# Kernel tuning notes

Hardware: AMD Instinct MI355X
Metric: run time of the kernel (lower is better)

## Reference

```python
import jax, jax.numpy as jnp
import numpy as np

B, D, FD, HW, NH, NC = 8, 384, 256, 64, 8, 4
NP = HW * HW
HD = D // NH


def _ln(x, g, b, eps=1e-5):
    m = jnp.mean(x, -1, keepdims=True)
    v = jnp.mean((x - m) ** 2, -1, keepdims=True)
    return (x - m) / jnp.sqrt(v + eps) * g + b


def _grn(x, g, b, eps=1e-6):
    # x: [B, D, H, W]; global L2 norm per channel over spatial dims
    gx = jnp.sqrt(jnp.sum(x * x, axis=(-2, -1), keepdims=True))  # [B,D,1,1]
    nx = gx / (jnp.mean(gx, axis=-3, keepdims=True) + eps)
    return (1.0 + g[:, None, None]) * (x * nx) + b[:, None, None] + x


def _adaln(x, film, W, bW, g, b):
    gb = film @ W.T + bW                       # [B, 2D]
    gamma, beta = jnp.split(gb, 2, axis=-1)
    return _grn(x, g, b) * (1.0 + gamma)[:, :, None, None] + beta[:, :, None, None]


def setup_inputs() -> dict:
    ks = jax.random.split(jax.random.key(0), 24)
    n = lambda k, s: jax.random.normal(k, s, jnp.float32)
    w = lambda k, o, i: n(k, (o, i)) * 0.02
    return {
        "image": n(ks[0], (B, D, HW, HW)),
        "film_vector": n(ks[1], (B, FD)),
        "perm": jax.random.permutation(ks[2], NP).astype(jnp.int32),
        "Wq": w(ks[3], D, D), "bq": jnp.zeros(D),
        "Wk": w(ks[4], D, D), "bk": jnp.zeros(D),
        "Wv": w(ks[5], D, D), "bv": jnp.zeros(D),
        "Wo": w(ks[6], D, D), "bo": jnp.zeros(D),
        "lnq_g": jnp.ones(D), "lnq_b": jnp.zeros(D),
        "lnk_g": jnp.ones(D), "lnk_b": jnp.zeros(D),
        "ada1_W": n(ks[7], (2 * D, FD)) * 0.001, "ada1_b": jnp.zeros(2 * D),
        "grn1_g": jnp.zeros(D), "grn1_b": jnp.zeros(D),
        "ada2_W": n(ks[8], (2 * D, FD)) * 0.001, "ada2_b": jnp.zeros(2 * D),
        "grn2_g": jnp.zeros(D), "grn2_b": jnp.zeros(D),
        "conv1_W": w(ks[9], 4 * D, D), "conv1_b": jnp.zeros(4 * D),
        "conv2_W": w(ks[10], D, 4 * D), "conv2_b": jnp.zeros(D),
        "cloud_scalar": jnp.ones(D),
        "ffn_scalar": jnp.ones(D),
        "final_scalar": jnp.ones(D) * 0.1,
        "num_clouds": NC,
    }


def reference(image, film_vector, perm, Wq, bq, Wk, bk, Wv, bv, Wo, bo,
              lnq_g, lnq_b, lnk_g, lnk_b, ada1_W, ada1_b, grn1_g, grn1_b,
              ada2_W, ada2_b, grn2_g, grn2_b, conv1_W, conv1_b, conv2_W, conv2_b,
              cloud_scalar, ffn_scalar, final_scalar, num_clouds):
    b, d, h, w = image.shape
    tp = h * w
    gs = tp // num_clouds

    # ---- cloud attention branch ----
    x = _adaln(image, film_vector, ada1_W, ada1_b, grn1_g, grn1_b)
    x_sh = x.reshape(b, d, tp)[:, :, perm]                       # shuffled pixels
    xg = x_sh.transpose(0, 2, 1).reshape(b * num_clouds, gs, d)  # [b*nc, gs, d]

    q = _ln(xg @ Wq.T + bq, lnq_g, lnq_b)
    k = _ln(xg @ Wk.T + bk, lnk_g, lnk_b)
    v = (xg @ Wv.T + bv).reshape(-1, gs, NH, HD)
    q = jax.nn.elu(q.reshape(-1, gs, NH, HD)) + 1.0
    k = jax.nn.elu(k.reshape(-1, gs, NH, HD)) + 1.0

    kv = jnp.einsum('bnhd,bnhe->bhde', k, v)                 # [b*nc, H, hd, hd]
    ksum = k.sum(axis=1)                                      # [b*nc, H, hd]
    num = jnp.einsum('bqhd,bhde->bqhe', q, kv)
    den = jnp.einsum('bqhd,bhd->bqh', q, ksum)[..., None] + 1e-8
    ao = (num / den).reshape(-1, gs, d) @ Wo.T + bo           # [b*nc, gs, d]

    ao = ao.reshape(b, num_clouds, gs, d).transpose(0, 3, 1, 2).reshape(b, d, tp)
    inv_perm = jnp.argsort(perm)
    ao = ao[:, :, inv_perm].reshape(b, d, h, w)

    wi = image + ao * cloud_scalar[:, None, None]

    # ---- FFN branch (1x1 convs) ----
    x2 = _adaln(wi, film_vector, ada2_W, ada2_b, grn2_g, grn2_b)
    h1 = jax.nn.silu(jnp.einsum('bdhw,ed->behw', x2, conv1_W) + conv1_b[:, None, None])
    fo = jnp.einsum('behw,de->bdhw', h1, conv2_W) + conv2_b[:, None, None]
    wi = wi + fo * ffn_scalar[:, None, None]

    return image + wi * final_scalar[:, None, None]
```

## Files before the change

kernel.cpp:

```cpp
#include <hip/hip_runtime.h>
#include <hip/hip_bf16.h>
#include <math.h>

#define BB      8
#define DD      384
#define FDIM    256
#define NPIX    4096
#define NHEAD   8
#define NCLOUD  4
#define HDIM    48
#define GSZ     1024
#define TT      (BB*NPIX)
#define DHID    (4*DD)
#define TD      1152

typedef __hip_bfloat16 bf16;
typedef __attribute__((ext_vector_type(8))) short bf16x8;
typedef __attribute__((ext_vector_type(4))) float f32x4;
typedef __attribute__((ext_vector_type(2))) unsigned int u32x2;

__device__ __forceinline__ float b2f(bf16 x){ return __bfloat162float(x); }
__device__ __forceinline__ bf16  f2b(float x){ return __float2bfloat16(x); }
__device__ __forceinline__ float lo2f(unsigned u){ union{unsigned i; float f;} c; c.i = u << 16; return c.f; }
__device__ __forceinline__ float hi2f(unsigned u){ union{unsigned i; float f;} c; c.i = u & 0xffff0000u; return c.f; }
__device__ __forceinline__ unsigned short f2bs(float x){ bf16 b = f2b(x); return *(unsigned short*)&b; }
__device__ __forceinline__ unsigned pack2(float a, float b){
    return (unsigned)f2bs(a) | ((unsigned)f2bs(b) << 16);
}

#if defined(__has_builtin)
#if __has_builtin(__builtin_amdgcn_global_load_lds)
#define USE_GLL 1
#endif
#endif
#ifndef USE_GLL
#define USE_GLL 0
#endif

typedef __attribute__((address_space(1))) void gas_t;
typedef __attribute__((address_space(3))) void las_t;
__device__ __forceinline__ void gload16(const void* g, void* l){
#if USE_GLL
    __builtin_amdgcn_global_load_lds((gas_t*)(void*)g, (las_t*)l, 16, 0, 0);
#else
    *(bf16x8*)l = *(const bf16x8*)g;
#endif
}

__device__ __forceinline__ float block_sum(float v, float* sm, int nthreads){
    #pragma unroll
    for (int o = 32; o > 0; o >>= 1) v += __shfl_down(v, o, 64);
    int nw = nthreads >> 6;
    __syncthreads();
    if ((threadIdx.x & 63) == 0) sm[threadIdx.x >> 6] = v;
    __syncthreads();
    float s = sm[0];
    for (int i = 1; i < nw; i++) s += sm[i];
    return s;
}

#define WSEG 147456
#define WBIG 589824
__global__ void prologue(const float* Wq, const float* Wk, const float* Wv, const float* Wo,
                         const float* W1, const float* W2, bf16* wb,
                         const float* film, const float* ada1_W, const float* ada1_b,
                         const float* ada2_W, const float* ada2_b, float* gb1, float* gb2,
                         const int* perm, int* invp,
                         const float* bq, const float* bk, const float* bv, float* bqkv,
                         float* gxsq, float* gxsq2){
    int blk = blockIdx.x, tid = threadIdx.x;
    if (blk < 6912){
        int i = blk*256 + tid;
        float v;
        if      (i <   WSEG) v = Wq[i];
        else if (i < 2*WSEG) v = Wk[i -   WSEG];
        else if (i < 3*WSEG) v = Wv[i - 2*WSEG];
        else if (i < 4*WSEG) v = Wo[i - 3*WSEG];
        else if (i < 4*WSEG + WBIG) v = W1[i - 4*WSEG];
        else v = W2[i - 4*WSEG - WBIG];
        wb[i] = f2b(v);
    } else if (blk < 6960){
        int idx = (blk-6912)*256 + tid;
        int which = idx / (BB*768);
        int r = idx % (BB*768);
        int bb = r / 768, j = r % 768;
        const float* W = which ? ada2_W : ada1_W;
        const float* bi = which ? ada2_b : ada1_b;
        const float* f = film + bb*FDIM;
        const float* w = W + (size_t)j*FDIM;
        float s = 0.f;
        for (int i = 0; i < FDIM; i++) s += f[i]*w[i];
        (which ? gb2 : gb1)[bb*768 + j] = s + bi[j];
    } else if (blk < 6976){
        int i = (blk-6960)*256 + tid;
        if (i < NPIX) invp[perm[i]] = i;
    } else if (blk < 6981){
        int i = (blk-6976)*256 + tid;
        if (i < 384) bqkv[i] = bq[i];
        else if (i < 768) bqkv[i] = bk[i-384];
        else if (i < 1152) bqkv[i] = bv[i-768];
    } else {
        int i = (blk-6981)*256 + tid;
        if (i < BB*DD){ gxsq[i] = 0.f; gxsq2[i] = 0.f; }
    }
}

__global__ void prep1(const float* img, bf16* imgT, float* gxsq){
    __shared__ float tile[32][33];
    __shared__ float red[32][8];
    int b = blockIdx.z, p0 = blockIdx.x*32, d0 = blockIdx.y*32;
    int tx = threadIdx.x, ty = threadIdx.y;
    #pragma unroll
    for (int i = 0; i < 32; i += 8)
        tile[ty+i][tx] = img[((size_t)b*DD + d0+ty+i)*NPIX + p0+tx];
    __syncthreads();
    #pragma unroll
    for (int i = 0; i < 32; i += 8){
        int p = p0 + ty + i;
        imgT[((size_t)(b<<12) + p)*DD + d0+tx] = f2b(tile[tx][ty+i]);
    }
    float s = 0.f;
    #pragma unroll
    for (int k = 0; k < 4; k++){ float v = tile[tx][ty*4 + k]; s += v*v; }
    red[tx][ty] = s;
    __syncthreads();
    if (ty == 0){
        float t2 = 0.f;
        #pragma unroll
        for (int k = 0; k < 8; k++) t2 += red[tx][k];
        atomicAdd(&gxsq[b*DD + d0+tx], t2);
    }
}

template<bool SQ>
__global__ void grn_nx(const float* gin, float* nx){
    __shared__ float sm[6];
    int b = blockIdx.x; int d = threadIdx.x;
    float g = gin[b*DD + d];
    if (SQ) g = sqrtf(g);
    float tot = block_sum(g, sm, 384);
    nx[b*DD + d] = g / (tot/(float)DD + 1e-6f);
}

__global__ __launch_bounds__(256) void adaln1_tok(const bf16* imgT, const float* nx,
                        const float* gg, const float* gbv, const float* gb,
                        const int* invp, bf16* xt){
    int t = blockIdx.x*4 + (threadIdx.x >> 6);
    int lane = threadIdx.x & 63;
    int b = t >> 12, p = t & 4095;
    int j = invp[p];
    const unsigned* src = (const unsigned*)(imgT + (size_t)t*DD);
    unsigned* dst = (unsigned*)(xt + ((size_t)(b<<12) + j)*DD);
    int d0 = lane*6;
    const float* nxp = nx + b*DD + d0;
    const float* g1 = gb + b*768 + d0;
    const float* g2 = gb + b*768 + 384 + d0;
    #pragma unroll
    for (int i = 0; i < 3; i++){
        unsigned u = src[lane*3 + i];
        float v0 = lo2f(u), v1 = hi2f(u);
        int dd0 = 2*i, dd1 = 2*i+1;
        float r0 = ((1.f + gg[d0+dd0])*(v0*nxp[dd0]) + gbv[d0+dd0] + v0)*(1.f + g1[dd0]) + g2[dd0];
        float r1 = ((1.f + gg[d0+dd1])*(v1*nxp[dd1]) + gbv[d0+dd1] + v1)*(1.f + g1[dd1]) + g2[dd1];
        dst[lane*3 + i] = pack2(r0, r1);
    }
}

__global__ __launch_bounds__(256) void adaln2_tok(const bf16* wi, const float* nx,
                        const float* gg, const float* gbv, const float* gb, bf16* xout){
    int t = blockIdx.x*4 + (threadIdx.x >> 6);
    int lane = threadIdx.x & 63;
    int b = t >> 12;
    const unsigned* src = (const unsigned*)(wi + (size_t)t*DD);
    unsigned* dst = (unsigned*)(xout + (size_t)t*DD);
    int d0 = lane*6;
    const float* nxp = nx + b*DD + d0;
    const float* g1 = gb + b*768 + d0;
    const float* g2 = gb + b*768 + 384 + d0;
    #pragma unroll
    for (int i = 0; i < 3; i++){
        unsigned u = src[lane*3 + i];
        float v0 = lo2f(u), v1 = hi2f(u);
        int dd0 = 2*i, dd1 = 2*i+1;
        float r0 = ((1.f + gg[d0+dd0])*(v0*nxp[dd0]) + gbv[d0+dd0] + v0)*(1.f + g1[dd0]) + g2[dd0];
        float r1 = ((1.f + gg[d0+dd1])*(v1*nxp[dd1]) + gbv[d0+dd1] + v1)*(1.f + g1[dd1]) + g2[dd1];
        dst[lane*3 + i] = pack2(r0, r1);
    }
}

template<int EPI>
__global__ __launch_bounds__(256, 2) void gemm_mfma(const bf16* __restrict__ A,
                          const bf16* __restrict__ W,
                          const float* __restrict__ bias,
                          bf16* __restrict__ C,
                          int M, int N, int K, const int* __restrict__ rowmap,
                          const bf16* __restrict__ imgT, const float* __restrict__ csc){
    __shared__ short lds_[36864];
    int tid  = threadIdx.x;
    int lane = tid & 63, wid = tid >> 6;
    int quad = lane >> 4, l16 = lane & 15;
    int wm = (wid >> 1) * 128, wn = (wid & 1) * 64;

    int v = blockIdx.y * gridDim.x + blockIdx.x;
    int xcd = v & 7, ii = v >> 3;
    int nby = gridDim.y;
    int by = xcd * (nby >> 3) + ii / gridDim.x;
    int bx = ii % gridDim.x;
    int m0 = by * 256, n0 = bx * 128;

    const bf16* sp[6]; int lof[6];
    #pragma unroll
    for (int it = 0; it < 6; it++){
        int s = tid + it*256;
        int half = s >> 10;
        int r = (s >> 2) & (half ? 127 : 255);
        int seg = (s & 3) ^ ((s >> 3) & 3);
        sp[it] = (half ? W + (size_t)(n0 + r)*K : A + (size_t)(m0 + r)*K) + seg*8;
        lof[it] = s*8;
    }
    int xorv = (quad ^ ((l16 >> 1) & 3)) * 8;

    int nk = K >> 5;
    #pragma unroll
    for (int it = 0; it < 6; it++) gload16(sp[it], lds_ + lof[it]);
    #pragma unroll
    for (int it = 0; it < 6; it++) gload16(sp[it] + 32, lds_ + 12288 + lof[it]);

    f32x4 acc[8][4] = {};
    for (int k = 0; k < nk; k++){
        if (k < nk-1) asm volatile("s_waitcnt vmcnt(6)" ::: "memory");
        else          asm volatile("s_waitcnt vmcnt(0)" ::: "memory");
        __builtin_amdgcn_s_barrier();
        __builtin_amdgcn_sched_barrier(0);
        if (k + 2 < nk){
            int koff = (k+2) * 32;
            int boff = ((k+2) % 3) * 12288;
            #pragma unroll
            for (int it = 0; it < 6; it++) gload16(sp[it] + koff, lds_ + boff + lof[it]);
        }
        const short* base = lds_ + (k % 3) * 12288;
        const short* a_ = base + (wm + l16)*32 + xorv;
        const short* w_ = base + 8192 + (wn + l16)*32 + xorv;
        bf16x8 af[8], wf[4];
        #pragma unroll
        for (int t = 0; t < 8; t++) af[t] = *(const bf16x8*)(void*)(a_ + t*512);
        #pragma unroll
        for (int t = 0; t < 4; t++) wf[t] = *(const bf16x8*)(void*)(w_ + t*512);
        #pragma unroll
        for (int i = 0; i < 8; i++)
            #pragma unroll
            for (int j2 = 0; j2 < 4; j2++)
                acc[i][j2] = __builtin_amdgcn_mfma_f32_16x16x32_bf16(wf[j2], af[i], acc[i][j2], 0, 0, 0);
    }
    int nbase = n0 + wn + quad*4;
    f32x4 bsv[4], csv[4];
    #pragma unroll
    for (int j2 = 0; j2 < 4; j2++) bsv[j2] = *(const f32x4*)(bias + nbase + j2*16);
    if (EPI == 2){
        #pragma unroll
        for (int j2 = 0; j2 < 4; j2++) csv[j2] = *(const f32x4*)(csc + nbase + j2*16);
    }
    #pragma unroll
    for (int i = 0; i < 8; i++){
        int row = m0 + wm + i*16 + l16;
        int grow = rowmap ? ((row & ~4095) | rowmap[row & 4095]) : row;
        bf16* cp = C + (size_t)grow*N + nbase;
        const bf16* ip = imgT + (size_t)grow*DD + nbase;
        #pragma unroll
        for (int j2 = 0; j2 < 4; j2++){
            float v0 = acc[i][j2][0] + bsv[j2][0];
            float v1 = acc[i][j2][1] + bsv[j2][1];
            float v2 = acc[i][j2][2] + bsv[j2][2];
            float v3 = acc[i][j2][3] + bsv[j2][3];
            if (EPI == 1){
                v0 = v0 / (1.f + __expf(-v0));
                v1 = v1 / (1.f + __expf(-v1));
                v2 = v2 / (1.f + __expf(-v2));
                v3 = v3 / (1.f + __expf(-v3));
            }
            if (EPI == 2){
                u32x2 iw = *(const u32x2*)(void*)(ip + j2*16);
                v0 = lo2f(iw.x) + v0*csv[j2][0];
                v1 = hi2f(iw.x) + v1*csv[j2][1];
                v2 = lo2f(iw.y) + v2*csv[j2][2];
                v3 = hi2f(iw.y) + v3*csv[j2][3];
            }
            u32x2 st;
            st.x = pack2(v0, v1);
            st.y = pack2(v2, v3);
            *(u32x2*)(void*)(cp + j2*16) = st;
        }
    }
}

__global__ __launch_bounds__(256) void ln_elu_qk(bf16* qkv,
                        const float* gq, const float* bq2,
                        const float* gk, const float* bk2){
    int r = blockIdx.x*4 + (threadIdx.x >> 6);
    int lane = threadIdx.x & 63;
    int t = r >> 1, which = r & 1;
    unsigned* row32 = (unsigned*)(qkv + (size_t)t*TD + which*384);
    const float* g = which ? gk : gq;
    const float* b = which ? bk2 : bq2;
    unsigned u[3];
    #pragma unroll
    for (int i = 0; i < 3; i++) u[i] = row32[lane*3 + i];
    float vv[6];
    #pragma unroll
    for (int i = 0; i < 3; i++){ vv[2*i] = lo2f(u[i]); vv[2*i+1] = hi2f(u[i]); }
    float s = 0.f;
    #pragma unroll
    for (int i = 0; i < 6; i++) s += vv[i];
    #pragma unroll
    for (int o = 32; o > 0; o >>= 1) s += __shfl_xor(s, o, 64);
    float mean = s / (float)DD;
    float s2 = 0.f;
    #pragma unroll
    for (int i = 0; i < 6; i++){ float d = vv[i]-mean; s2 += d*d; }
    #pragma unroll
    for (int o = 32; o > 0; o >>= 1) s2 += __shfl_xor(s2, o, 64);
    float rstd = rsqrtf(s2/(float)DD + 1e-5f);
    int d0 = lane*6;
    #pragma unroll
    for (int i = 0; i < 3; i++){
        float y0 = (vv[2*i]-mean)*rstd*g[d0+2*i] + b[d0+2*i];
        float y1 = (vv[2*i+1]-mean)*rstd*g[d0+2*i+1] + b[d0+2*i+1];
        y0 = (y0 > 0.f) ? y0 : expm1f(y0);
        y1 = (y1 > 0.f) ? y1 : expm1f(y1);
        row32[lane*3 + i] = pack2(y0 + 1.f, y1 + 1.f);
    }
}

__global__ __launch_bounds__(256) void kv_ksum_part(const bf16* qkv, float* kvp, float* ksp){
    int bch = blockIdx.x >> 3, sub = blockIdx.x & 7;
    int bc = bch >> 3, h = bch & 7;
    __shared__ float ks[16][49];
    __shared__ float vs[16][49];
    int eg = (threadIdx.x >> 4) * 3;
    int fg = (threadIdx.x & 15) * 3;
    float acc[3][3] = {};
    float ksacc[3] = {};
    int nbase = bc*GSZ + sub*128;
    for (int n0 = 0; n0 < 128; n0 += 16){
        for (int i = threadIdx.x; i < 16*48; i += 256){
            int n = i/48, e = i%48;
            size_t base = (size_t)(nbase + n0 + n)*TD + h*HDIM;
            ks[n][e] = b2f(qkv[base + 384 + e]);
            vs[n][e] = b2f(qkv[base + 768 + e]);
        }
        __syncthreads();
        #pragma unroll 4
        for (int n = 0; n < 16; n++){
            float ka[3], vb[3];
            #pragma unroll
            for (int i = 0; i < 3; i++){ ka[i] = ks[n][eg+i]; vb[i] = vs[n][fg+i]; }
            #pragma unroll
            for (int i = 0; i < 3; i++)
                #pragma unroll
                for (int j = 0; j < 3; j++)
                    acc[i][j] += ka[i]*vb[j];
            if ((threadIdx.x & 15) == 0){
                #pragma unroll
                for (int i = 0; i < 3; i++) ksacc[i] += ka[i];
            }
        }
        __syncthreads();
    }
    float* kvo = kvp + (size_t)blockIdx.x*2304;
    #pragma unroll
    for (int i = 0; i < 3; i++)
        #pragma unroll
        for (int j = 0; j < 3; j++)
            kvo[(eg+i)*48 + fg+j] = acc[i][j];
    if ((threadIdx.x & 15) == 0){
        #pragma unroll
        for (int i = 0; i < 3; i++) ksp[(size_t)blockIdx.x*48 + eg+i] = ksacc[i];
    }
}

__global__ void kv_reduce(const float* kvp, const float* ksp, float* kv, float* ksum){
    int idx = blockIdx.x*256 + threadIdx.x;
    if (idx < 256*2304){
        int bch = idx / 2304, r = idx - bch*2304;
        const float* p = kvp + (size_t)bch*8*2304 + r;
        float s = 0.f;
        #pragma unroll
        for (int u = 0; u < 8; u++) s += p[u*2304];
        kv[idx] = s;
    } else if (idx < 256*2304 + 256*48){
        int k2 = idx - 256*2304;
        int bch = k2 / 48, r = k2 - bch*48;
        const float* p = ksp + (size_t)bch*8*48 + r;
        float s = 0.f;
        #pragma unroll
        for (int u = 0; u < 8; u++) s += p[u*48];
        ksum[k2] = s;
    }
}

__global__ __launch_bounds__(256) void attn_apply(const bf16* __restrict__ qkv,
                                                  const float* __restrict__ kv,
                                                  const float* __restrict__ ksum,
                                                  bf16* __restrict__ out){
    __shared__ __align__(16) bf16 Wm[64][72];
    int bch = blockIdx.x >> 2, rs = blockIdx.x & 3;
    int bc = bch >> 3, h = bch & 7;
    int tid = threadIdx.x;
    int lane = tid & 63, w = tid >> 6;
    int l16 = lane & 15, quad = lane >> 4;

    for (int i = tid; i < 64*72; i += 256) ((unsigned short*)Wm)[i] = 0;
    __syncthreads();
    const float* kvh = kv + (size_t)bch*(HDIM*HDIM);
    for (int i = tid; i < HDIM*HDIM; i += 256){
        int e = i / HDIM, f = i - e*HDIM;
        Wm[f][e] = f2b(kvh[i]);
    }
    if (tid < HDIM) Wm[HDIM][tid] = f2b(ksum[(size_t)bch*HDIM + tid]);
    __syncthreads();

    bf16x8 bw[4][2];
    #pragma unroll
    for (int n = 0; n < 4; n++){
        bw[n][0] = *(const bf16x8*)(void*)&Wm[n*16 + l16][quad*8];
        bw[n][1] = *(const bf16x8*)(void*)&Wm[n*16 + l16][32 + quad*8];
    }

    int rowbase0 = bc*GSZ + rs*256 + w*64;
    #pragma unroll
    for (int frag = 0; frag < 4; frag++){
        int arow = rowbase0 + frag*16 + l16;
        const bf16* qp = qkv + (size_t)arow*TD + h*HDIM;
        bf16x8 a0 = *(const bf16x8*)(void*)(qp + quad*8);
        bf16x8 a1 = {};
        if (quad < 2) a1 = *(const bf16x8*)(void*)(qp + 32 + quad*8);
        f32x4 acc[4] = {};
        #pragma unroll
        for (int n = 0; n < 4; n++){
            acc[n] = __builtin_amdgcn_mfma_f32_16x16x32_bf16(a0, bw[n][0], acc[n], 0, 0, 0);
            acc[n] = __builtin_amdgcn_mfma_f32_16x16x32_bf16(a1, bw[n][1], acc[n], 0, 0, 0);
        }
        int orow0 = rowbase0 + frag*16 + quad*4;
        #pragma unroll
        for (int r = 0; r < 4; r++){
            float den = __shfl(acc[3][r], quad*16, 64);
            float inv = 1.f / (den + 1e-8f);
            bf16* op = out + (size_t)(orow0 + r)*DD + h*HDIM + l16;
            op[0]  = f2b(acc[0][r]*inv);
            op[16] = f2b(acc[1][r]*inv);
            op[32] = f2b(acc[2][r]*inv);
        }
    }
}

__global__ __launch_bounds__(256) void colsq(const bf16* wi, float* gxsq2){
    __shared__ float red[4][DD];
    int wave = threadIdx.x >> 6, lane = threadIdx.x & 63;
    int t0 = blockIdx.x*128 + wave*32;
    int b = (blockIdx.x*128) >> 12;
    int d0 = lane*6;
    float acc[6] = {};
    for (int it = 0; it < 32; it++){
        const unsigned* pw = (const unsigned*)(wi + (size_t)(t0 + it)*DD);
        #pragma unroll
        for (int i = 0; i < 3; i++){
            unsigned u = pw[lane*3 + i];
            float v0 = lo2f(u), v1 = hi2f(u);
            acc[2*i]   += v0*v0;
            acc[2*i+1] += v1*v1;
        }
    }
    #pragma unroll
    for (int i = 0; i < 6; i++) red[wave][d0+i] = acc[i];
    __syncthreads();
    for (int d = threadIdx.x; d < DD; d += 256){
        float s = red[0][d] + red[1][d] + red[2][d] + red[3][d];
        atomicAdd(&gxsq2[b*DD + d], s);
    }
}

__global__ void final_out(const float* img, const bf16* wi, const bf16* fot,
                          const float* ffs, const float* fins, float* out){
    __shared__ float tile[32][33];
    int b = blockIdx.z, p0 = blockIdx.x*32, d0 = blockIdx.y*32;
    int tx = threadIdx.x, ty = threadIdx.y;
    #pragma unroll
    for (int i = 0; i < 32; i += 8){
        size_t t = (size_t)(b<<12) + p0+ty+i;
        tile[ty+i][tx] = b2f(wi[t*DD + d0+tx]) + b2f(fot[t*DD + d0+tx])*ffs[d0+tx];
    }
    __syncthreads();
    #pragma unroll
    for (int i = 0; i < 32; i += 8){
        int d = d0 + ty + i;
        size_t o = ((size_t)b*DD + d)*NPIX + p0+tx;
        out[o] = img[o] + tile[tx][ty+i]*fins[d];
    }
}

extern "C" void kernel_launch(void* const* d_in, const int* in_sizes, int n_in,
                              void* d_out, int out_size, void* d_ws, size_t ws_size,
                              hipStream_t stream){
    const float* image   = (const float*)d_in[0];
    const float* film    = (const float*)d_in[1];
    const int*   perm    = (const int*)  d_in[2];
    const float* Wq      = (const float*)d_in[3];
    const float* bq      = (const float*)d_in[4];
    const float* Wk      = (const float*)d_in[5];
    const float* bk      = (const float*)d_in[6];
    const float* Wv      = (const float*)d_in[7];
    const float* bv      = (const float*)d_in[8];
    const float* Wo      = (const float*)d_in[9];
    const float* bo      = (const float*)d_in[10];
    const float* lnq_g   = (const float*)d_in[11];
    const float* lnq_b   = (const float*)d_in[12];
    const float* lnk_g   = (const float*)d_in[13];
    const float* lnk_b   = (const float*)d_in[14];
    const float* ada1_W  = (const float*)d_in[15];
    const float* ada1_b  = (const float*)d_in[16];
    const float* grn1_g  = (const float*)d_in[17];
    const float* grn1_b  = (const float*)d_in[18];
    const float* ada2_W  = (const float*)d_in[19];
    const float* ada2_b  = (const float*)d_in[20];
    const float* grn2_g  = (const float*)d_in[21];
    const float* grn2_b  = (const float*)d_in[22];
    const float* conv1_W = (const float*)d_in[23];
    const float* conv1_b = (const float*)d_in[24];
    const float* conv2_W = (const float*)d_in[25];
    const float* conv2_b = (const float*)d_in[26];
    const float* cs      = (const float*)d_in[27];
    const float* ffs     = (const float*)d_in[28];
    const float* fins    = (const float*)d_in[29];
    float* out = (float*)d_out;

    char* m = (char*)d_ws;
    float* gb1     = (float*)m;  m += (size_t)BB*768*4;
    float* gb2     = (float*)m;  m += (size_t)BB*768*4;
    int*   invp    = (int*)m;    m += (size_t)NPIX*4;
    float* gxsq    = (float*)m;  m += (size_t)BB*DD*4;
    float* gxsq2   = (float*)m;  m += (size_t)BB*DD*4;
    float* nx      = (float*)m;  m += (size_t)BB*DD*4;
    float* kvbuf   = (float*)m;  m += (size_t)256*HDIM*HDIM*4;
    float* ksumbuf = (float*)m;  m += (size_t)256*HDIM*4;
    float* kvp     = (float*)m;  m += (size_t)2048*2304*4;
    float* ksp     = (float*)m;  m += (size_t)2048*48*4;
    float* bqkv    = (float*)m;  m += (size_t)TD*4;
    bf16*  wb      = (bf16*)m;   m += (size_t)(4*WSEG + 2*WBIG)*2;
    bf16*  wqkv = wb;
    bf16*  wbo  = wb + 3*WSEG;
    bf16*  wb1  = wb + 4*WSEG, *wb2 = wb + 4*WSEG + WBIG;
    bf16* imgT = (bf16*)m;       m += (size_t)TT*DD*2;
    bf16* qkv = (bf16*)m;        m += (size_t)TT*TD*2;
    bf16* obf = (bf16*)m;        m += (size_t)TT*DD*2;
    bf16* abf = (bf16*)m;        m += (size_t)TT*DD*2;
    bf16* wi  = (bf16*)m;        m += (size_t)TT*DD*2;
    bf16* H1  = qkv;
    (void)obf;

    prologue<<<6993, 256, 0, stream>>>(Wq, Wk, Wv, Wo, conv1_W, conv2_W, wb,
                                       film, ada1_W, ada1_b, ada2_W, ada2_b, gb1, gb2,
                                       perm, invp, bq, bk, bv, bqkv, gxsq, gxsq2);

    prep1<<<dim3(128,12,BB), dim3(32,8), 0, stream>>>(image, imgT, gxsq);
    grn_nx<true><<<BB, DD, 0, stream>>>(gxsq, nx);
    adaln1_tok<<<TT/4, 256, 0, stream>>>(imgT, nx, grn1_g, grn1_b, gb1, invp, abf);
    gemm_mfma<0><<<dim3(9,128), 256, 0, stream>>>(abf, wqkv, bqkv, qkv, TT, TD, DD, nullptr, nullptr, nullptr);
    ln_elu_qk<<<2*TT/4, 256, 0, stream>>>(qkv, lnq_g, lnq_b, lnk_g, lnk_b);
    kv_ksum_part<<<2048, 256, 0, stream>>>(qkv, kvp, ksp);
    kv_reduce<<<2352, 256, 0, stream>>>(kvp, ksp, kvbuf, ksumbuf);
    attn_apply<<<1024, 256, 0, stream>>>(qkv, kvbuf, ksumbuf, abf);
    gemm_mfma<2><<<dim3(3,128), 256, 0, stream>>>(abf, wbo, bo, wi, TT, DD, DD, perm, imgT, cs);
    colsq<<<BB*32, 256, 0, stream>>>(wi, gxsq2);

    grn_nx<true><<<BB, DD, 0, stream>>>(gxsq2, nx);
    adaln2_tok<<<TT/4, 256, 0, stream>>>(wi, nx, grn2_g, grn2_b, gb2, abf);
    gemm_mfma<1><<<dim3(12,128), 256, 0, stream>>>(abf, wb1, conv1_b, H1, TT, DHID, DD, nullptr, nullptr, nullptr);
    gemm_mfma<0><<<dim3(3,128), 256, 0, stream>>>(H1, wb2, conv2_b, abf, TT, DD, DHID, nullptr, nullptr, nullptr);
    final_out<<<dim3(128,12,BB), dim3(32,8), 0, stream>>>(image, wi, abf, ffs, fins, out);
}
```

Measured before the change: 533.3 us.

## Compute KV outer products with MFMA and add smaller-M GEMM tile variant

Replaces the scalar FP32 kv/ksum partial kernel and its separate reduction kernel with one MFMA kernel per (cloud, head). K and V are transposed into LDS, and a row of ones is appended to V so ksum comes out of the same matmul. The four wave partials are then reduced in LDS, which removes the partial buffers and a launch. It also templates the GEMM on a 128-row M tile and uses it for the QKV and output-projection GEMMs, doubling their grid to improve occupancy and wave balance. The trade-off is extra LDS transposes and bf16 MFMA accumulation of K·V, and only 256 blocks for the kv stage.

```diff
diff --git a/kernel.cpp b/kernel.cpp
--- a/kernel.cpp
+++ b/kernel.cpp
@@ -188,32 +188,36 @@
     }
 }
 
-template<int EPI>
+template<int EPI, int BIGM>
 __global__ __launch_bounds__(256, 2) void gemm_mfma(const bf16* __restrict__ A,
                           const bf16* __restrict__ W,
                           const float* __restrict__ bias,
                           bf16* __restrict__ C,
                           int M, int N, int K, const int* __restrict__ rowmap,
                           const bf16* __restrict__ imgT, const float* __restrict__ csc){
-    __shared__ short lds_[36864];
+    constexpr int BM   = BIGM ? 256 : 128;
+    constexpr int NCH  = BIGM ? 6 : 4;
+    constexpr int BUFS = BIGM ? 12288 : 8192;
+    constexpr int WOFF = BIGM ? 8192 : 4096;
+    constexpr int NA   = BIGM ? 8 : 4;
+    __shared__ short lds_[3*BUFS];
     int tid  = threadIdx.x;
     int lane = tid & 63, wid = tid >> 6;
     int quad = lane >> 4, l16 = lane & 15;
-    int wm = (wid >> 1) * 128, wn = (wid & 1) * 64;
+    int wm = (wid >> 1) * (BIGM ? 128 : 64), wn = (wid & 1) * 64;
 
     int v = blockIdx.y * gridDim.x + blockIdx.x;
     int xcd = v & 7, ii = v >> 3;
-    int nby = gridDim.y;
-    int by = xcd * (nby >> 3) + ii / gridDim.x;
+    int by = xcd * (gridDim.y >> 3) + ii / gridDim.x;
     int bx = ii % gridDim.x;
-    int m0 = by * 256, n0 = bx * 128;
-
-    const bf16* sp[6]; int lof[6];
-    #pragma unroll
-    for (int it = 0; it < 6; it++){
+    int m0 = by * BM, n0 = bx * 128;
+
+    const bf16* sp[NCH]; int lof[NCH];
+    #pragma unroll
+    for (int it = 0; it < NCH; it++){
         int s = tid + it*256;
-        int half = s >> 10;
-        int r = (s >> 2) & (half ? 127 : 255);
+        int half = (s >= BM*4) ? 1 : 0;
+        int r = (s >> 2) & (half ? 127 : (BM-1));
         int seg = (s & 3) ^ ((s >> 3) & 3);
         sp[it] = (half ? W + (size_t)(n0 + r)*K : A + (size_t)(m0 + r)*K) + seg*8;
         lof[it] = s*8;
@@ -222,32 +226,36 @@
 
     int nk = K >> 5;
     #pragma unroll
-    for (int it = 0; it < 6; it++) gload16(sp[it], lds_ + lof[it]);
-    #pragma unroll
-    for (int it = 0; it < 6; it++) gload16(sp[it] + 32, lds_ + 12288 + lof[it]);
-
-    f32x4 acc[8][4] = {};
+    for (int it = 0; it < NCH; it++) gload16(sp[it], lds_ + lof[it]);
+    #pragma unroll
+    for (int it = 0; it < NCH; it++) gload16(sp[it] + 32, lds_ + BUFS + lof[it]);
+
+    f32x4 acc[NA][4] = {};
     for (int k = 0; k < nk; k++){
-        if (k < nk-1) asm volatile("s_waitcnt vmcnt(6)" ::: "memory");
-        else          asm volatile("s_waitcnt vmcnt(0)" ::: "memory");
+        if (k < nk-1){
+            if constexpr (BIGM) asm volatile("s_waitcnt vmcnt(6)" ::: "memory");
+            else                asm volatile("s_waitcnt vmcnt(4)" ::: "memory");
+        } else {
+            asm volatile("s_waitcnt vmcnt(0)" ::: "memory");
+        }
         __builtin_amdgcn_s_barrier();
         __builtin_amdgcn_sched_barrier(0);
         if (k + 2 < nk){
             int koff = (k+2) * 32;
-            int boff = ((k+2) % 3) * 12288;
-            #pragma unroll
-            for (int it = 0; it < 6; it++) gload16(sp[it] + koff, lds_ + boff + lof[it]);
-        }
-        const short* base = lds_ + (k % 3) * 12288;
+            int boff = ((k+2) % 3) * BUFS;
+            #pragma unroll
+            for (int it = 0; it < NCH; it++) gload16(sp[it] + koff, lds_ + boff + lof[it]);
+        }
+        const short* base = lds_ + (k % 3) * BUFS;
         const short* a_ = base + (wm + l16)*32 + xorv;
-        const short* w_ = base + 8192 + (wn + l16)*32 + xorv;
-        bf16x8 af[8], wf[4];
-        #pragma unroll
-        for (int t = 0; t < 8; t++) af[t] = *(const bf16x8*)(void*)(a_ + t*512);
+        const short* w_ = base + WOFF + (wn + l16)*32 + xorv;
+        bf16x8 af[NA], wf[4];
+        #pragma unroll
+        for (int t = 0; t < NA; t++) af[t] = *(const bf16x8*)(void*)(a_ + t*512);
         #pragma unroll
         for (int t = 0; t < 4; t++) wf[t] = *(const bf16x8*)(void*)(w_ + t*512);
         #pragma unroll
-        for (int i = 0; i < 8; i++)
+        for (int i = 0; i < NA; i++)
             #pragma unroll
             for (int j2 = 0; j2 < 4; j2++)
                 acc[i][j2] = __builtin_amdgcn_mfma_f32_16x16x32_bf16(wf[j2], af[i], acc[i][j2], 0, 0, 0);
@@ -261,7 +269,7 @@
         for (int j2 = 0; j2 < 4; j2++) csv[j2] = *(const f32x4*)(csc + nbase + j2*16);
     }
     #pragma unroll
-    for (int i = 0; i < 8; i++){
+    for (int i = 0; i < NA; i++){
         int row = m0 + wm + i*16 + l16;
         int grow = rowmap ? ((row & ~4095) | rowmap[row & 4095]) : row;
         bf16* cp = C + (size_t)grow*N + nbase;
@@ -331,70 +339,76 @@
     }
 }
 
-__global__ __launch_bounds__(256) void kv_ksum_part(const bf16* qkv, float* kvp, float* ksp){
-    int bch = blockIdx.x >> 3, sub = blockIdx.x & 7;
+__global__ __launch_bounds__(256) void kv_mfma(const bf16* __restrict__ qkv,
+                                               float* __restrict__ kv,
+                                               float* __restrict__ ksum){
+    __shared__ __align__(16) short lds_[32256];
+    float* red = (float*)lds_;
+    constexpr int KCH = 48*72;
+    constexpr int VCH = 64*72;
+    constexpr int VBASE = 4*KCH;
+    int tid = threadIdx.x;
+    int lane = tid & 63, w = tid >> 6;
+    int l16 = lane & 15, quad = lane >> 4;
+    int bch = blockIdx.x;
     int bc = bch >> 3, h = bch & 7;
-    __shared__ float ks[16][49];
-    __shared__ float vs[16][49];
-    int eg = (threadIdx.x >> 4) * 3;
-    int fg = (threadIdx.x & 15) * 3;
-    float acc[3][3] = {};
-    float ksacc[3] = {};
-    int nbase = bc*GSZ + sub*128;
-    for (int n0 = 0; n0 < 128; n0 += 16){
-        for (int i = threadIdx.x; i < 16*48; i += 256){
-            int n = i/48, e = i%48;
-            size_t base = (size_t)(nbase + n0 + n)*TD + h*HDIM;
-            ks[n][e] = b2f(qkv[base + 384 + e]);
-            vs[n][e] = b2f(qkv[base + 768 + e]);
+
+    f32x4 acc[3][4] = {};
+    for (int it = 0; it < 4; it++){
+        int nl = tid & 63;
+        const bf16* tp = qkv + (size_t)(bc*GSZ + it*256 + tid)*TD + h*HDIM;
+        bf16x8 kf[6], vf[6];
+        #pragma unroll
+        for (int c = 0; c < 6; c++){
+            kf[c] = *(const bf16x8*)(void*)(tp + 384 + c*8);
+            vf[c] = *(const bf16x8*)(void*)(tp + 768 + c*8);
         }
         __syncthreads();
-        #pragma unroll 4
-        for (int n = 0; n < 16; n++){
-            float ka[3], vb[3];
-            #pragma unroll
-            for (int i = 0; i < 3; i++){ ka[i] = ks[n][eg+i]; vb[i] = vs[n][fg+i]; }
+        short* kt = lds_ + w*KCH;
+        short* vt = lds_ + VBASE + w*VCH;
+        #pragma unroll
+        for (int c = 0; c < 6; c++)
+            #pragma unroll
+            for (int j = 0; j < 8; j++){
+                kt[(c*8+j)*72 + nl] = kf[c][j];
+                vt[(c*8+j)*72 + nl] = vf[c][j];
+            }
+        vt[48*72 + nl] = (short)0x3F80;
+        __syncthreads();
+        const short* ka = lds_ + w*KCH;
+        const short* va = lds_ + VBASE + w*VCH;
+        #pragma unroll
+        for (int ks = 0; ks < 2; ks++){
+            int n0 = ks*32 + quad*8;
+            bf16x8 af[3], bfr[4];
+            #pragma unroll
+            for (int i = 0; i < 3; i++)  af[i]  = *(const bf16x8*)(void*)(ka + (i*16+l16)*72 + n0);
+            #pragma unroll
+            for (int j2 = 0; j2 < 4; j2++) bfr[j2] = *(const bf16x8*)(void*)(va + (j2*16+l16)*72 + n0);
             #pragma unroll
             for (int i = 0; i < 3; i++)
                 #pragma unroll
-                for (int j = 0; j < 3; j++)
-                    acc[i][j] += ka[i]*vb[j];
-            if ((threadIdx.x & 15) == 0){
-                #pragma unroll
-                for (int i = 0; i < 3; i++) ksacc[i] += ka[i];
+                for (int j2 = 0; j2 < 4; j2++)
+                    acc[i][j2] = __builtin_amdgcn_mfma_f32_16x16x32_bf16(af[i], bfr[j2], acc[i][j2], 0, 0, 0);
+        }
+    }
+    __syncthreads();
+    #pragma unroll
+    for (int i = 0; i < 3; i++)
+        #pragma unroll
+        for (int j2 = 0; j2 < 4; j2++)
+            #pragma unroll
+            for (int r = 0; r < 4; r++){
+                int d = i*16 + quad*4 + r;
+                int e = j2*16 + l16;
+                red[w*3072 + d*64 + e] = acc[i][j2][r];
             }
-        }
-        __syncthreads();
-    }
-    float* kvo = kvp + (size_t)blockIdx.x*2304;
-    #pragma unroll
-    for (int i = 0; i < 3; i++)
-        #pragma unroll
-        for (int j = 0; j < 3; j++)
-            kvo[(eg+i)*48 + fg+j] = acc[i][j];
-    if ((threadIdx.x & 15) == 0){
-        #pragma unroll
-        for (int i = 0; i < 3; i++) ksp[(size_t)blockIdx.x*48 + eg+i] = ksacc[i];
-    }
-}
-
-__global__ void kv_reduce(const float* kvp, const float* ksp, float* kv, float* ksum){
-    int idx = blockIdx.x*256 + threadIdx.x;
-    if (idx < 256*2304){
-        int bch = idx / 2304, r = idx - bch*2304;
-        const float* p = kvp + (size_t)bch*8*2304 + r;
-        float s = 0.f;
-        #pragma unroll
-        for (int u = 0; u < 8; u++) s += p[u*2304];
-        kv[idx] = s;
-    } else if (idx < 256*2304 + 256*48){
-        int k2 = idx - 256*2304;
-        int bch = k2 / 48, r = k2 - bch*48;
-        const float* p = ksp + (size_t)bch*8*48 + r;
-        float s = 0.f;
-        #pragma unroll
-        for (int u = 0; u < 8; u++) s += p[u*48];
-        ksum[k2] = s;
+    __syncthreads();
+    for (int i = tid; i < 3072; i += 256){
+        float s = red[i] + red[3072+i] + red[6144+i] + red[9216+i];
+        int d = i >> 6, e = i & 63;
+        if (e < 48)       kv[(size_t)bch*2304 + d*48 + e] = s;
+        else if (e == 48) ksum[(size_t)bch*48 + d] = s;
     }
 }
 
@@ -542,8 +556,6 @@
     float* nx      = (float*)m;  m += (size_t)BB*DD*4;
     float* kvbuf   = (float*)m;  m += (size_t)256*HDIM*HDIM*4;
     float* ksumbuf = (float*)m;  m += (size_t)256*HDIM*4;
-    float* kvp     = (float*)m;  m += (size_t)2048*2304*4;
-    float* ksp     = (float*)m;  m += (size_t)2048*48*4;
     float* bqkv    = (float*)m;  m += (size_t)TD*4;
     bf16*  wb      = (bf16*)m;   m += (size_t)(4*WSEG + 2*WBIG)*2;
     bf16*  wqkv = wb;
@@ -564,17 +576,16 @@
     prep1<<<dim3(128,12,BB), dim3(32,8), 0, stream>>>(image, imgT, gxsq);
     grn_nx<true><<<BB, DD, 0, stream>>>(gxsq, nx);
     adaln1_tok<<<TT/4, 256, 0, stream>>>(imgT, nx, grn1_g, grn1_b, gb1, invp, abf);
-    gemm_mfma<0><<<dim3(9,128), 256, 0, stream>>>(abf, wqkv, bqkv, qkv, TT, TD, DD, nullptr, nullptr, nullptr);
+    gemm_mfma<0,0><<<dim3(9,256), 256, 0, stream>>>(abf, wqkv, bqkv, qkv, TT, TD, DD, nullptr, nullptr, nullptr);
     ln_elu_qk<<<2*TT/4, 256, 0, stream>>>(qkv, lnq_g, lnq_b, lnk_g, lnk_b);
-    kv_ksum_part<<<2048, 256, 0, stream>>>(qkv, kvp, ksp);
-    kv_reduce<<<2352, 256, 0, stream>>>(kvp, ksp, kvbuf, ksumbuf);
+    kv_mfma<<<256, 256, 0, stream>>>(qkv, kvbuf, ksumbuf);
     attn_apply<<<1024, 256, 0, stream>>>(qkv, kvbuf, ksumbuf, abf);
-    gemm_mfma<2><<<dim3(3,128), 256, 0, stream>>>(abf, wbo, bo, wi, TT, DD, DD, perm, imgT, cs);
+    gemm_mfma<2,0><<<dim3(3,256), 256, 0, stream>>>(abf, wbo, bo, wi, TT, DD, DD, perm, imgT, cs);
     colsq<<<BB*32, 256, 0, stream>>>(wi, gxsq2);
 
     grn_nx<true><<<BB, DD, 0, stream>>>(gxsq2, nx);
     adaln2_tok<<<TT/4, 256, 0, stream>>>(wi, nx, grn2_g, grn2_b, gb2, abf);
-    gemm_mfma<1><<<dim3(12,128), 256, 0, stream>>>(abf, wb1, conv1_b, H1, TT, DHID, DD, nullptr, nullptr, nullptr);
-    gemm_mfma<0><<<dim3(3,128), 256, 0, stream>>>(H1, wb2, conv2_b, abf, TT, DD, DHID, nullptr, nullptr, nullptr);
+    gemm_mfma<1,1><<<dim3(12,128), 256, 0, stream>>>(abf, wb1, conv1_b, H1, TT, DHID, DD, nullptr, nullptr, nullptr);
+    gemm_mfma<0,1><<<dim3(3,128), 256, 0, stream>>>(H1, wb2, conv2_b, abf, TT, DD, DHID, nullptr, nullptr, nullptr);
     final_out<<<dim3(128,12,BB), dim3(32,8), 0, stream>>>(image, wi, abf, ffs, fins, out);
 }
```

Result: faster. 508.4 us (-4.7%).
